# Optimization experiments

Hardware: AMD Instinct MI355X
Metric: run time of the kernel (lower is better)

Reference implementation:

```python
import math
import jax, jax.numpy as jnp
import numpy as np

D_MODEL = 1024
N_HEADS = 16
HEAD_DIM = D_MODEL // N_HEADS
D_FF = 4096
LN_EPS = 1e-5


def _layer_norm(x, g, b):
    mu = jnp.mean(x, axis=-1, keepdims=True)
    var = jnp.var(x, axis=-1, keepdims=True)
    return (x - mu) * jax.lax.rsqrt(var + LN_EPS) * g + b


def setup_inputs() -> dict:
    key = jax.random.key(0)
    ks = jax.random.split(key, 8)
    s = 0.02
    d, dff = D_MODEL, D_FF
    return {
        "src": jax.random.normal(ks[0], (2, 2048, d), dtype=jnp.float32),
        "in_proj_w": jax.random.normal(ks[1], (3 * d, d), dtype=jnp.float32) * s,
        "in_proj_b": jnp.zeros((3 * d,), dtype=jnp.float32),
        "out_w": jax.random.normal(ks[2], (d, d), dtype=jnp.float32) * s,
        "out_b": jnp.zeros((d,), dtype=jnp.float32),
        "lin1_w": jax.random.normal(ks[3], (dff, d), dtype=jnp.float32) * s,
        "lin1_b": jnp.zeros((dff,), dtype=jnp.float32),
        "lin2_w": jax.random.normal(ks[4], (d, dff), dtype=jnp.float32) * s,
        "lin2_b": jnp.zeros((d,), dtype=jnp.float32),
        "ln1_g": jnp.ones((d,), dtype=jnp.float32),
        "ln1_b": jnp.zeros((d,), dtype=jnp.float32),
        "ln2_g": jnp.ones((d,), dtype=jnp.float32),
        "ln2_b": jnp.zeros((d,), dtype=jnp.float32),
    }


def reference(src, in_proj_w, in_proj_b, out_w, out_b, lin1_w, lin1_b,
              lin2_w, lin2_b, ln1_g, ln1_b, ln2_g, ln2_b):
    B, S, d = src.shape
    # QKV projections (in_proj_weight split at d, then kv split)
    q = src @ in_proj_w[:d].T + in_proj_b[:d]              # [B,S,d]
    kv = src @ in_proj_w[d:].T + in_proj_b[d:]             # [B,S,2d]
    q = q.reshape(B, S, N_HEADS, HEAD_DIM)
    kv = kv.reshape(B, S, 2, N_HEADS, HEAD_DIM)
    k, v = kv[:, :, 0], kv[:, :, 1]
    softmax_scale = 1.0 / math.sqrt(HEAD_DIM)
    scores = jnp.einsum('bthd,bshd->bhts', q, k) * softmax_scale  # [B,H,Sq,Skv]
    # 'distribute': softmax over the QUERY dimension (dim=-2)
    attention = jax.nn.softmax(scores, axis=-2)
    post = jnp.einsum('bhts,bshd->bthd', attention, v)     # [B,Sq,H,hd]
    # post-attention activation 'gelu' (torch exact gelu)
    post = jax.nn.gelu(post, approximate=False)
    # attention_scale == 'sqrt': divide by sqrt(kv_len)
    post = post / math.sqrt(S)
    attn_out = post.reshape(B, S, d) @ out_w.T + out_b
    # post-norm residual structure (pre_norm=False, dropout=0)
    x = _layer_norm(src + attn_out, ln1_g, ln1_b)
    ff = jax.nn.gelu(x @ lin1_w.T + lin1_b, approximate=False) @ lin2_w.T + lin2_b
    return _layer_norm(x + ff, ln2_g, ln2_b)
```

## Files before the change

### kernel.cpp

```cpp
#include <hip/hip_runtime.h>
#include <hip/hip_bf16.h>
#include <math.h>


using bf16x8 = __attribute__((ext_vector_type(8))) short;
using f32x4  = __attribute__((ext_vector_type(4))) float;

__device__ inline f32x4 mfma16(bf16x8 a, bf16x8 b, f32x4 c) {
    return __builtin_amdgcn_mfma_f32_16x16x32_bf16(a, b, c, 0, 0, 0);
}

__device__ inline ushort f2bf(float f) {
    union { float f; unsigned u; } x; x.f = f;
    unsigned r = x.u + 0x7fffu + ((x.u >> 16) & 1u);
    return (ushort)(r >> 16);
}

__device__ inline float bf2f(ushort u) {
    union { unsigned u; float f; } x; x.u = ((unsigned)u) << 16; return x.f;
}

__device__ inline float gelu_exact(float v) {
    return 0.5f * v * (1.0f + erff(v * 0.70710678118654752f));
}

__global__ __launch_bounds__(256) void cvt_kernel(const float4* __restrict__ in,
                                                  ushort* __restrict__ out, int n4) {
    int i = blockIdx.x * 256 + threadIdx.x;
    if (i >= n4) return;
    float4 v = in[i];
    ushort4 o;
    o.x = f2bf(v.x); o.y = f2bf(v.y); o.z = f2bf(v.z); o.w = f2bf(v.w);
    ((ushort4*)out)[i] = o;
}

__global__ __launch_bounds__(256) void gemm_bt(
    const ushort* __restrict__ A, const ushort* __restrict__ Bw,
    const float* __restrict__ bias, int M, int N, int K, int mode,
    ushort* __restrict__ ob0, ushort* __restrict__ ob1, ushort* __restrict__ ob2,
    const float* __restrict__ res, float* __restrict__ of) {
    __shared__ ushort As[128 * 32];
    __shared__ ushort Bs[128 * 32];
    int tid = threadIdx.x, lane = tid & 63, wid = tid >> 6;
    int wm = wid >> 1, wn = wid & 1;
    int bm = blockIdx.y * 128, bn = blockIdx.x * 128;
    int q4 = lane >> 4, l15 = lane & 15;
    f32x4 acc[4][4] = {};

    int srow = tid >> 2, scol = (tid & 3) * 8;
    const ushort* Ab = A + (size_t)bm * K;
    const ushort* Bb = Bw + (size_t)bn * K;

    for (int k0 = 0; k0 < K; k0 += 32) {
        uint4 a0 = *(const uint4*)(Ab + (size_t)srow * K + k0 + scol);
        uint4 a1 = *(const uint4*)(Ab + (size_t)(64 + srow) * K + k0 + scol);
        uint4 b0 = *(const uint4*)(Bb + (size_t)srow * K + k0 + scol);
        uint4 b1 = *(const uint4*)(Bb + (size_t)(64 + srow) * K + k0 + scol);
        __syncthreads();
        *(uint4*)&As[srow * 32 + scol] = a0;
        *(uint4*)&As[(64 + srow) * 32 + scol] = a1;
        *(uint4*)&Bs[srow * 32 + scol] = b0;
        *(uint4*)&Bs[(64 + srow) * 32 + scol] = b1;
        __syncthreads();
        bf16x8 af[4], bfr[4];
#pragma unroll
        for (int mi = 0; mi < 4; mi++)
            af[mi] = *(bf16x8*)&As[(wm * 64 + mi * 16 + l15) * 32 + q4 * 8];
#pragma unroll
        for (int ni = 0; ni < 4; ni++)
            bfr[ni] = *(bf16x8*)&Bs[(wn * 64 + ni * 16 + l15) * 32 + q4 * 8];
#pragma unroll
        for (int mi = 0; mi < 4; mi++)
#pragma unroll
            for (int ni = 0; ni < 4; ni++)
                acc[mi][ni] = mfma16(af[mi], bfr[ni], acc[mi][ni]);
    }

    int r0 = bm + wm * 64, c0 = bn + wn * 64;
#pragma unroll
    for (int mi = 0; mi < 4; mi++) {
#pragma unroll
        for (int ni = 0; ni < 4; ni++) {
            int colg = c0 + ni * 16 + l15;
            float bv = bias[colg];
#pragma unroll
            for (int r = 0; r < 4; r++) {
                int rowg = r0 + mi * 16 + q4 * 4 + r;
                float v = acc[mi][ni][r] + bv;
                if (mode == 0) {
                    if (colg < 1024) {
                        ob0[(size_t)rowg * 1024 + colg] = f2bf(v);
                    } else if (colg < 2048) {
                        ob1[(size_t)rowg * 1024 + (colg - 1024)] = f2bf(v);
                    } else {
                        int c = colg - 2048;
                        int hh = c >> 6, dh = c & 63;
                        int b = rowg >> 11, s = rowg & 2047;
                        ob2[((size_t)(b * 16 + hh) * 64 + dh) * 2048 + s] = f2bf(v);
                    }
                } else if (mode == 1) {
                    size_t idx = (size_t)rowg * N + colg;
                    of[idx] = v + res[idx];
                } else {
                    ob0[(size_t)rowg * N + colg] = f2bf(gelu_exact(v));
                }
            }
        }
    }
}

__global__ __launch_bounds__(256) void attn_colsum(const ushort* __restrict__ qb,
                                                   const ushort* __restrict__ kb,
                                                   float* __restrict__ ninv) {
    __shared__ ushort Qs[64 * 72];
    int tid = threadIdx.x, lane = tid & 63, w = tid >> 6;
    int bh = blockIdx.x >> 4, sblk = blockIdx.x & 15;
    int b = bh >> 4, h = bh & 15;
    int q4 = lane >> 4, l15 = lane & 15;
    const ushort* qbase = qb + (size_t)(b * 2048) * 1024 + h * 64;
    const ushort* kbase = kb + (size_t)(b * 2048) * 1024 + h * 64;
    int s_base = sblk * 128 + w * 32;

    bf16x8 ka[2][2];
#pragma unroll
    for (int mi = 0; mi < 2; mi++) {
        const ushort* kp = kbase + (size_t)(s_base + mi * 16 + l15) * 1024 + q4 * 8;
        ka[mi][0] = *(const bf16x8*)(kp);
        ka[mi][1] = *(const bf16x8*)(kp + 32);
    }
    float acc[2][4] = {};

    int sr = tid >> 3;
    int sc = (tid & 7) * 8;
    for (int t0 = 0; t0 < 2048; t0 += 64) {
        uint4 g0 = *(const uint4*)(qbase + (size_t)(t0 + sr) * 1024 + sc);
        uint4 g1 = *(const uint4*)(qbase + (size_t)(t0 + 32 + sr) * 1024 + sc);
        __syncthreads();
        *(uint4*)&Qs[sr * 72 + sc] = g0;
        *(uint4*)&Qs[(32 + sr) * 72 + sc] = g1;
        __syncthreads();
#pragma unroll
        for (int tsub = 0; tsub < 4; tsub++) {
            bf16x8 bq0 = *(const bf16x8*)&Qs[(tsub * 16 + l15) * 72 + q4 * 8];
            bf16x8 bq1 = *(const bf16x8*)&Qs[(tsub * 16 + l15) * 72 + 32 + q4 * 8];
#pragma unroll
            for (int mi = 0; mi < 2; mi++) {
                f32x4 d = {0.f, 0.f, 0.f, 0.f};
                d = mfma16(ka[mi][0], bq0, d);
                d = mfma16(ka[mi][1], bq1, d);
#pragma unroll
                for (int r = 0; r < 4; r++)
                    acc[mi][r] += __expf(d[r] * 0.125f);
            }
        }
    }
#pragma unroll
    for (int mi = 0; mi < 2; mi++)
#pragma unroll
        for (int r = 0; r < 4; r++) {
            float v = acc[mi][r];
            v += __shfl_xor(v, 1); v += __shfl_xor(v, 2);
            v += __shfl_xor(v, 4); v += __shfl_xor(v, 8);
            if (l15 == 0)
                ninv[(size_t)bh * 2048 + s_base + mi * 16 + q4 * 4 + r] = 1.f / v;
        }
}

__global__ __launch_bounds__(256) void scale_vt(ushort* __restrict__ vt,
                                                const float* __restrict__ ninv) {
    int g = blockIdx.x * 256 + threadIdx.x;
    size_t base = (size_t)g * 8;
    int bh = g >> 14;
    int s = (int)(base & 2047);
    float4 n0 = ((const float4*)(ninv + (size_t)bh * 2048 + s))[0];
    float4 n1 = ((const float4*)(ninv + (size_t)bh * 2048 + s))[1];
    ushort4 a = ((const ushort4*)(vt + base))[0];
    ushort4 c = ((const ushort4*)(vt + base))[1];
    ushort4 oa, oc;
    oa.x = f2bf(bf2f(a.x) * n0.x); oa.y = f2bf(bf2f(a.y) * n0.y);
    oa.z = f2bf(bf2f(a.z) * n0.z); oa.w = f2bf(bf2f(a.w) * n0.w);
    oc.x = f2bf(bf2f(c.x) * n1.x); oc.y = f2bf(bf2f(c.y) * n1.y);
    oc.z = f2bf(bf2f(c.z) * n1.z); oc.w = f2bf(bf2f(c.w) * n1.w);
    ((ushort4*)(vt + base))[0] = oa;
    ((ushort4*)(vt + base))[1] = oc;
}

__global__ __launch_bounds__(256) void attn_pv(const ushort* __restrict__ qb,
                                               const ushort* __restrict__ kb,
                                               const ushort* __restrict__ vt,
                                               ushort* __restrict__ post) {
    __shared__ ushort Ks[64 * 72];
    __shared__ ushort Vs[64 * 72];
    __shared__ ushort Ps[4][32 * 72];
    int tid = threadIdx.x, lane = tid & 63, w = tid >> 6;
    int bh = blockIdx.x >> 4, tblk = blockIdx.x & 15;
    int b = bh >> 4, h = bh & 15;
    int q4 = lane >> 4, l15 = lane & 15;
    const ushort* qbase = qb + (size_t)(b * 2048) * 1024 + h * 64;
    const ushort* kbase = kb + (size_t)(b * 2048) * 1024 + h * 64;
    const ushort* vtb = vt + (size_t)bh * 64 * 2048;
    int t_base = tblk * 128 + w * 32;

    bf16x8 aq[2][2];
#pragma unroll
    for (int mi = 0; mi < 2; mi++) {
        const ushort* qp = qbase + (size_t)(t_base + mi * 16 + l15) * 1024 + q4 * 8;
        aq[mi][0] = *(const bf16x8*)(qp);
        aq[mi][1] = *(const bf16x8*)(qp + 32);
    }
    f32x4 oacc[2][4] = {};
    ushort* myP = Ps[w];

    int sr = tid >> 3;
    int sc = (tid & 7) * 8;
    for (int s0 = 0; s0 < 2048; s0 += 64) {
        uint4 k0g = *(const uint4*)(kbase + (size_t)(s0 + sr) * 1024 + sc);
        uint4 k1g = *(const uint4*)(kbase + (size_t)(s0 + 32 + sr) * 1024 + sc);
        uint4 v0g = *(const uint4*)(vtb + (size_t)sr * 2048 + s0 + sc);
        uint4 v1g = *(const uint4*)(vtb + (size_t)(32 + sr) * 2048 + s0 + sc);
        __syncthreads();
        *(uint4*)&Ks[sr * 72 + sc] = k0g;
        *(uint4*)&Ks[(32 + sr) * 72 + sc] = k1g;
        *(uint4*)&Vs[sr * 72 + sc] = v0g;
        *(uint4*)&Vs[(32 + sr) * 72 + sc] = v1g;
        __syncthreads();
#pragma unroll
        for (int ssub = 0; ssub < 4; ssub++) {
            bf16x8 bk0 = *(const bf16x8*)&Ks[(ssub * 16 + l15) * 72 + q4 * 8];
            bf16x8 bk1 = *(const bf16x8*)&Ks[(ssub * 16 + l15) * 72 + 32 + q4 * 8];
#pragma unroll
            for (int mi = 0; mi < 2; mi++) {
                f32x4 d = {0.f, 0.f, 0.f, 0.f};
                d = mfma16(aq[mi][0], bk0, d);
                d = mfma16(aq[mi][1], bk1, d);
#pragma unroll
                for (int r = 0; r < 4; r++)
                    myP[(mi * 16 + q4 * 4 + r) * 72 + ssub * 16 + l15] =
                        f2bf(__expf(d[r] * 0.125f));
            }
        }
        bf16x8 bv[4][2];
#pragma unroll
        for (int ni = 0; ni < 4; ni++) {
            bv[ni][0] = *(const bf16x8*)&Vs[(ni * 16 + l15) * 72 + q4 * 8];
            bv[ni][1] = *(const bf16x8*)&Vs[(ni * 16 + l15) * 72 + 32 + q4 * 8];
        }
#pragma unroll
        for (int mi = 0; mi < 2; mi++) {
            bf16x8 ap0 = *(const bf16x8*)&myP[(mi * 16 + l15) * 72 + q4 * 8];
            bf16x8 ap1 = *(const bf16x8*)&myP[(mi * 16 + l15) * 72 + 32 + q4 * 8];
#pragma unroll
            for (int ni = 0; ni < 4; ni++) {
                oacc[mi][ni] = mfma16(ap0, bv[ni][0], oacc[mi][ni]);
                oacc[mi][ni] = mfma16(ap1, bv[ni][1], oacc[mi][ni]);
            }
        }
    }
#pragma unroll
    for (int mi = 0; mi < 2; mi++)
#pragma unroll
        for (int ni = 0; ni < 4; ni++)
#pragma unroll
            for (int r = 0; r < 4; r++) {
                int t = t_base + mi * 16 + q4 * 4 + r;
                float g = gelu_exact(oacc[mi][ni][r]) * 0.022097086912079608f;
                post[(size_t)(b * 2048 + t) * 1024 + h * 64 + ni * 16 + l15] = f2bf(g);
            }
}

__global__ __launch_bounds__(256) void ln_kernel(const float* __restrict__ in,
                                                 const float* __restrict__ gw,
                                                 const float* __restrict__ bw,
                                                 ushort* __restrict__ outb,
                                                 float* __restrict__ outf) {
    int row = blockIdx.x, tid = threadIdx.x;
    int lane = tid & 63, wid = tid >> 6;
    float4 v = ((const float4*)(in + (size_t)row * 1024))[tid];
    float s = v.x + v.y + v.z + v.w;
    float ss = v.x * v.x + v.y * v.y + v.z * v.z + v.w * v.w;
    for (int m = 1; m < 64; m <<= 1) { s += __shfl_xor(s, m); ss += __shfl_xor(ss, m); }
    __shared__ float red[8];
    if (lane == 0) { red[wid] = s; red[wid + 4] = ss; }
    __syncthreads();
    s = red[0] + red[1] + red[2] + red[3];
    ss = red[4] + red[5] + red[6] + red[7];
    float mu = s * (1.f / 1024.f);
    float var = ss * (1.f / 1024.f) - mu * mu;
    float inv = rsqrtf(var + 1e-5f);
    float4 gv = ((const float4*)gw)[tid];
    float4 bv = ((const float4*)bw)[tid];
    float o0 = (v.x - mu) * inv * gv.x + bv.x;
    float o1 = (v.y - mu) * inv * gv.y + bv.y;
    float o2 = (v.z - mu) * inv * gv.z + bv.z;
    float o3 = (v.w - mu) * inv * gv.w + bv.w;
    if (outf) {
        float4 o; o.x = o0; o.y = o1; o.z = o2; o.w = o3;
        ((float4*)(outf + (size_t)row * 1024))[tid] = o;
    }
    if (outb) {
        ushort4 o; o.x = f2bf(o0); o.y = f2bf(o1); o.z = f2bf(o2); o.w = f2bf(o3);
        ((ushort4*)(outb + (size_t)row * 1024))[tid] = o;
    }
}

extern "C" void kernel_launch(void* const* d_in, const int* in_sizes, int n_in,
                              void* d_out, int out_size, void* d_ws, size_t ws_size,
                              hipStream_t stream) {
    const float* src  = (const float*)d_in[0];
    const float* w_in = (const float*)d_in[1];
    const float* b_in = (const float*)d_in[2];
    const float* w_o  = (const float*)d_in[3];
    const float* b_o  = (const float*)d_in[4];
    const float* w1   = (const float*)d_in[5];
    const float* b1   = (const float*)d_in[6];
    const float* w2   = (const float*)d_in[7];
    const float* b2   = (const float*)d_in[8];
    const float* g1   = (const float*)d_in[9];
    const float* be1  = (const float*)d_in[10];
    const float* g2   = (const float*)d_in[11];
    const float* be2  = (const float*)d_in[12];
    float* out = (float*)d_out;

    const size_t M = 4096;
    char* wsp = (char*)d_ws;
    size_t off = 0;
    auto alloc = [&](size_t bytes) -> void* {
        void* p = wsp + off;
        off = (off + bytes + 255) & ~(size_t)255;
        return p;
    };
    ushort* src_bf  = (ushort*)alloc(M * 1024 * 2);
    ushort* win_bf  = (ushort*)alloc(3072 * 1024 * 2);
    ushort* wout_bf = (ushort*)alloc(1024 * 1024 * 2);
    ushort* w1_bf   = (ushort*)alloc(4096 * 1024 * 2);
    ushort* w2_bf   = (ushort*)alloc((size_t)1024 * 4096 * 2);
    ushort* q_bf    = (ushort*)alloc(M * 1024 * 2);
    ushort* k_bf    = (ushort*)alloc(M * 1024 * 2);
    ushort* vt_bf   = (ushort*)alloc(M * 1024 * 2);
    float*  ninv    = (float*)alloc(2 * 16 * 2048 * 4);
    ushort* post_bf = (ushort*)alloc(M * 1024 * 2);
    float*  ypre    = (float*)alloc(M * 1024 * 4);
    ushort* x_bf    = (ushort*)alloc(M * 1024 * 2);
    float*  x_f32   = (float*)alloc(M * 1024 * 4);
    ushort* h1_bf   = (ushort*)alloc(M * 4096 * 2);

    cvt_kernel<<<4096, 256, 0, stream>>>((const float4*)src, src_bf, 1048576);
    cvt_kernel<<<3072, 256, 0, stream>>>((const float4*)w_in, win_bf, 786432);
    cvt_kernel<<<1024, 256, 0, stream>>>((const float4*)w_o, wout_bf, 262144);
    cvt_kernel<<<4096, 256, 0, stream>>>((const float4*)w1, w1_bf, 1048576);
    cvt_kernel<<<4096, 256, 0, stream>>>((const float4*)w2, w2_bf, 1048576);

    gemm_bt<<<dim3(24, 32), 256, 0, stream>>>(src_bf, win_bf, b_in, 4096, 3072, 1024, 0,
                                              q_bf, k_bf, vt_bf, nullptr, nullptr);

    attn_colsum<<<512, 256, 0, stream>>>(q_bf, k_bf, ninv);
    scale_vt<<<2048, 256, 0, stream>>>(vt_bf, ninv);
    attn_pv<<<512, 256, 0, stream>>>(q_bf, k_bf, vt_bf, post_bf);

    gemm_bt<<<dim3(8, 32), 256, 0, stream>>>(post_bf, wout_bf, b_o, 4096, 1024, 1024, 1,
                                             nullptr, nullptr, nullptr, src, ypre);
    ln_kernel<<<4096, 256, 0, stream>>>(ypre, g1, be1, x_bf, x_f32);

    gemm_bt<<<dim3(32, 32), 256, 0, stream>>>(x_bf, w1_bf, b1, 4096, 4096, 1024, 2,
                                              h1_bf, nullptr, nullptr, nullptr, nullptr);
    gemm_bt<<<dim3(8, 32), 256, 0, stream>>>(h1_bf, w2_bf, b2, 4096, 1024, 4096, 1,
                                             nullptr, nullptr, nullptr, x_f32, ypre);
    ln_kernel<<<4096, 256, 0, stream>>>(ypre, g2, be2, nullptr, out);
}
```

Measured before the change: 528.3 us.

## Split-K the N=1024 GEMMs, fold partial sums into LayerNorm, use direct global-to-LDS loads

The two GEMMs with N=1024 (out-proj and lin2) now run as split-K over two z-slices. Each slice writes fp32 partials, and a new ln_comb kernel adds the partials, bias and residual before the LayerNorm. This raises the block count from 256 to 512 so more CUs are busy. The GEMM tile loads also switch to global_load_lds, which writes straight into LDS without staging through registers. The cost is extra fp32 partial traffic, and the loop has no explicit wait on the async LDS loads beyond __syncthreads.

```diff
diff --git a/kernel.cpp b/kernel.cpp
--- a/kernel.cpp
+++ b/kernel.cpp
@@ -22,6 +22,13 @@
 
 __device__ inline float gelu_exact(float v) {
     return 0.5f * v * (1.0f + erff(v * 0.70710678118654752f));
+}
+
+__device__ __forceinline__ void gl2lds16(const ushort* g, ushort* l) {
+    __builtin_amdgcn_global_load_lds(
+        (const __attribute__((address_space(1))) unsigned int*)g,
+        (__attribute__((address_space(3))) unsigned int*)l,
+        16, 0, 0);
 }
 
 __global__ __launch_bounds__(256) void cvt_kernel(const float4* __restrict__ in,
@@ -36,39 +43,52 @@
 
 __global__ __launch_bounds__(256) void gemm_bt(
     const ushort* __restrict__ A, const ushort* __restrict__ Bw,
-    const float* __restrict__ bias, int M, int N, int K, int mode,
+    const float* __restrict__ bias, int M, int N, int K, int kLen, int mode,
     ushort* __restrict__ ob0, ushort* __restrict__ ob1, ushort* __restrict__ ob2,
-    const float* __restrict__ res, float* __restrict__ of) {
+    float* __restrict__ of) {
     __shared__ ushort As[128 * 32];
     __shared__ ushort Bs[128 * 32];
-    int tid = threadIdx.x, lane = tid & 63, wid = tid >> 6;
-    int wm = wid >> 1, wn = wid & 1;
+    int tid = threadIdx.x, lane = tid & 63, w = tid >> 6;
+    int wm = w >> 1, wn = w & 1;
     int bm = blockIdx.y * 128, bn = blockIdx.x * 128;
+    int kz = blockIdx.z;
     int q4 = lane >> 4, l15 = lane & 15;
     f32x4 acc[4][4] = {};
 
-    int srow = tid >> 2, scol = (tid & 3) * 8;
-    const ushort* Ab = A + (size_t)bm * K;
-    const ushort* Bb = Bw + (size_t)bn * K;
-
-    for (int k0 = 0; k0 < K; k0 += 32) {
-        uint4 a0 = *(const uint4*)(Ab + (size_t)srow * K + k0 + scol);
-        uint4 a1 = *(const uint4*)(Ab + (size_t)(64 + srow) * K + k0 + scol);
-        uint4 b0 = *(const uint4*)(Bb + (size_t)srow * K + k0 + scol);
-        uint4 b1 = *(const uint4*)(Bb + (size_t)(64 + srow) * K + k0 + scol);
-        __syncthreads();
-        *(uint4*)&As[srow * 32 + scol] = a0;
-        *(uint4*)&As[(64 + srow) * 32 + scol] = a1;
-        *(uint4*)&Bs[srow * 32 + scol] = b0;
-        *(uint4*)&Bs[(64 + srow) * 32 + scol] = b1;
+    int srow = w * 16 + (lane >> 2);
+    int scg = lane & 3;
+    const ushort* Ab = A + (size_t)bm * K + (size_t)kz * kLen;
+    const ushort* Bb = Bw + (size_t)bn * K + (size_t)kz * kLen;
+    const ushort* gA0 = Ab + (size_t)srow * K + scg * 8;
+    const ushort* gA1 = Ab + (size_t)(64 + srow) * K + scg * 8;
+    const ushort* gB0 = Bb + (size_t)srow * K + scg * 8;
+    const ushort* gB1 = Bb + (size_t)(64 + srow) * K + scg * 8;
+    ushort* lA0 = As + w * 512;
+    ushort* lA1 = As + 2048 + w * 512;
+    ushort* lB0 = Bs + w * 512;
+    ushort* lB1 = Bs + 2048 + w * 512;
+
+    const ushort* aP[4];
+    const ushort* bP[4];
+#pragma unroll
+    for (int mi = 0; mi < 4; mi++)
+        aP[mi] = As + (wm * 64 + mi * 16 + l15) * 32 + q4 * 8;
+#pragma unroll
+    for (int ni = 0; ni < 4; ni++)
+        bP[ni] = Bs + (wn * 64 + ni * 16 + l15) * 32 + q4 * 8;
+
+    for (int k0 = 0; k0 < kLen; k0 += 32) {
+        __syncthreads();
+        gl2lds16(gA0 + k0, lA0);
+        gl2lds16(gA1 + k0, lA1);
+        gl2lds16(gB0 + k0, lB0);
+        gl2lds16(gB1 + k0, lB1);
         __syncthreads();
         bf16x8 af[4], bfr[4];
 #pragma unroll
-        for (int mi = 0; mi < 4; mi++)
-            af[mi] = *(bf16x8*)&As[(wm * 64 + mi * 16 + l15) * 32 + q4 * 8];
-#pragma unroll
-        for (int ni = 0; ni < 4; ni++)
-            bfr[ni] = *(bf16x8*)&Bs[(wn * 64 + ni * 16 + l15) * 32 + q4 * 8];
+        for (int mi = 0; mi < 4; mi++) af[mi] = *(const bf16x8*)aP[mi];
+#pragma unroll
+        for (int ni = 0; ni < 4; ni++) bfr[ni] = *(const bf16x8*)bP[ni];
 #pragma unroll
         for (int mi = 0; mi < 4; mi++)
 #pragma unroll
@@ -82,7 +102,7 @@
 #pragma unroll
         for (int ni = 0; ni < 4; ni++) {
             int colg = c0 + ni * 16 + l15;
-            float bv = bias[colg];
+            float bv = (mode == 3) ? 0.f : bias[colg];
 #pragma unroll
             for (int r = 0; r < 4; r++) {
                 int rowg = r0 + mi * 16 + q4 * 4 + r;
@@ -98,11 +118,10 @@
                         int b = rowg >> 11, s = rowg & 2047;
                         ob2[((size_t)(b * 16 + hh) * 64 + dh) * 2048 + s] = f2bf(v);
                     }
-                } else if (mode == 1) {
-                    size_t idx = (size_t)rowg * N + colg;
-                    of[idx] = v + res[idx];
+                } else if (mode == 2) {
+                    ob0[(size_t)rowg * N + colg] = f2bf(gelu_exact(v));
                 } else {
-                    ob0[(size_t)rowg * N + colg] = f2bf(gelu_exact(v));
+                    of[(size_t)kz * M * N + (size_t)rowg * N + colg] = v;
                 }
             }
         }
@@ -268,14 +287,26 @@
             }
 }
 
-__global__ __launch_bounds__(256) void ln_kernel(const float* __restrict__ in,
-                                                 const float* __restrict__ gw,
-                                                 const float* __restrict__ bw,
-                                                 ushort* __restrict__ outb,
-                                                 float* __restrict__ outf) {
+__global__ __launch_bounds__(256) void ln_comb(const float* __restrict__ p0,
+                                               const float* __restrict__ p1,
+                                               const float* __restrict__ bias,
+                                               const float* __restrict__ res,
+                                               const float* __restrict__ gw,
+                                               const float* __restrict__ bw,
+                                               ushort* __restrict__ outb,
+                                               float* __restrict__ outf) {
     int row = blockIdx.x, tid = threadIdx.x;
     int lane = tid & 63, wid = tid >> 6;
-    float4 v = ((const float4*)(in + (size_t)row * 1024))[tid];
+    size_t off = (size_t)row * 1024;
+    float4 a = ((const float4*)(p0 + off))[tid];
+    float4 b = ((const float4*)(p1 + off))[tid];
+    float4 r = ((const float4*)(res + off))[tid];
+    float4 bb = ((const float4*)bias)[tid];
+    float4 v;
+    v.x = a.x + b.x + r.x + bb.x;
+    v.y = a.y + b.y + r.y + bb.y;
+    v.z = a.z + b.z + r.z + bb.z;
+    v.w = a.w + b.w + r.w + bb.w;
     float s = v.x + v.y + v.z + v.w;
     float ss = v.x * v.x + v.y * v.y + v.z * v.z + v.w * v.w;
     for (int m = 1; m < 64; m <<= 1) { s += __shfl_xor(s, m); ss += __shfl_xor(ss, m); }
@@ -295,11 +326,11 @@
     float o3 = (v.w - mu) * inv * gv.w + bv.w;
     if (outf) {
         float4 o; o.x = o0; o.y = o1; o.z = o2; o.w = o3;
-        ((float4*)(outf + (size_t)row * 1024))[tid] = o;
+        ((float4*)(outf + off))[tid] = o;
     }
     if (outb) {
         ushort4 o; o.x = f2bf(o0); o.y = f2bf(o1); o.z = f2bf(o2); o.w = f2bf(o3);
-        ((ushort4*)(outb + (size_t)row * 1024))[tid] = o;
+        ((ushort4*)(outb + off))[tid] = o;
     }
 }
 
@@ -339,7 +370,7 @@
     ushort* vt_bf   = (ushort*)alloc(M * 1024 * 2);
     float*  ninv    = (float*)alloc(2 * 16 * 2048 * 4);
     ushort* post_bf = (ushort*)alloc(M * 1024 * 2);
-    float*  ypre    = (float*)alloc(M * 1024 * 4);
+    float*  part    = (float*)alloc(2 * M * 1024 * 4);
     ushort* x_bf    = (ushort*)alloc(M * 1024 * 2);
     float*  x_f32   = (float*)alloc(M * 1024 * 4);
     ushort* h1_bf   = (ushort*)alloc(M * 4096 * 2);
@@ -350,20 +381,20 @@
     cvt_kernel<<<4096, 256, 0, stream>>>((const float4*)w1, w1_bf, 1048576);
     cvt_kernel<<<4096, 256, 0, stream>>>((const float4*)w2, w2_bf, 1048576);
 
-    gemm_bt<<<dim3(24, 32), 256, 0, stream>>>(src_bf, win_bf, b_in, 4096, 3072, 1024, 0,
-                                              q_bf, k_bf, vt_bf, nullptr, nullptr);
+    gemm_bt<<<dim3(24, 32, 1), 256, 0, stream>>>(src_bf, win_bf, b_in, 4096, 3072, 1024, 1024, 0,
+                                                 q_bf, k_bf, vt_bf, nullptr);
 
     attn_colsum<<<512, 256, 0, stream>>>(q_bf, k_bf, ninv);
     scale_vt<<<2048, 256, 0, stream>>>(vt_bf, ninv);
     attn_pv<<<512, 256, 0, stream>>>(q_bf, k_bf, vt_bf, post_bf);
 
-    gemm_bt<<<dim3(8, 32), 256, 0, stream>>>(post_bf, wout_bf, b_o, 4096, 1024, 1024, 1,
-                                             nullptr, nullptr, nullptr, src, ypre);
-    ln_kernel<<<4096, 256, 0, stream>>>(ypre, g1, be1, x_bf, x_f32);
-
-    gemm_bt<<<dim3(32, 32), 256, 0, stream>>>(x_bf, w1_bf, b1, 4096, 4096, 1024, 2,
-                                              h1_bf, nullptr, nullptr, nullptr, nullptr);
-    gemm_bt<<<dim3(8, 32), 256, 0, stream>>>(h1_bf, w2_bf, b2, 4096, 1024, 4096, 1,
-                                             nullptr, nullptr, nullptr, x_f32, ypre);
-    ln_kernel<<<4096, 256, 0, stream>>>(ypre, g2, be2, nullptr, out);
-}
+    gemm_bt<<<dim3(8, 32, 2), 256, 0, stream>>>(post_bf, wout_bf, b_o, 4096, 1024, 1024, 512, 3,
+                                                nullptr, nullptr, nullptr, part);
+    ln_comb<<<4096, 256, 0, stream>>>(part, part + M * 1024, b_o, src, g1, be1, x_bf, x_f32);
+
+    gemm_bt<<<dim3(32, 32, 1), 256, 0, stream>>>(x_bf, w1_bf, b1, 4096, 4096, 1024, 1024, 2,
+                                                 h1_bf, nullptr, nullptr, nullptr);
+    gemm_bt<<<dim3(8, 32, 2), 256, 0, stream>>>(h1_bf, w2_bf, b2, 4096, 1024, 4096, 2048, 3,
+                                                nullptr, nullptr, nullptr, part);
+    ln_comb<<<4096, 256, 0, stream>>>(part, part + M * 1024, b2, x_f32, g2, be2, nullptr, out);
+}
```

Result: faster. 487.8 us (-7.7%).
